# Kernel optimization log

Measured on AMD Instinct MI355X. Metric: run time of the kernel, lower is better.

## Reference

```python
import jax, jax.numpy as jnp
import numpy as np

N_NODES = 100000
N_EDGES = 1600000
D = 128  # in_feats = n_hidden = out_feats


def _linear_params(key, d_in, d_out):
    kw, kb = jax.random.split(key)
    scale = 1.0 / np.sqrt(d_in)
    W = jax.random.uniform(kw, (d_in, d_out), jnp.float32, -scale, scale)
    b = jax.random.uniform(kb, (d_out,), jnp.float32, -scale, scale)
    return W, b


def setup_inputs() -> dict:
    key = jax.random.key(0)
    keys = jax.random.split(key, 8)
    x = jax.random.normal(keys[0], (N_NODES, D), jnp.float32)
    edge_index = jax.random.randint(keys[1], (2, N_EDGES), 0, N_NODES, jnp.int64)
    inp = {"x": x, "edge_index": edge_index}
    for l in range(3):
        W1, b1 = _linear_params(keys[2 + 2 * l], D, D)
        W2, b2 = _linear_params(keys[3 + 2 * l], D, D)
        inp[f"W1_{l}"] = W1
        inp[f"b1_{l}"] = b1
        inp[f"W2_{l}"] = W2
        inp[f"b2_{l}"] = b2
    return inp


def _gin_conv(x, src, dst, W1, b1, W2, b2):
    # GINConv: MLP((1+eps)*x + sum_{j->i} x_j), eps=0
    agg = jax.ops.segment_sum(x[src], dst, num_segments=N_NODES)
    h = agg + x
    h = jnp.maximum(h @ W1 + b1, 0.0)
    return h @ W2 + b2


def reference(x, edge_index, W1_0, b1_0, W2_0, b2_0,
              W1_1, b1_1, W2_1, b2_1, W1_2, b1_2, W2_2, b2_2):
    src, dst = edge_index[0], edge_index[1]
    # layer 0 (loop body): conv -> relu
    x = jnp.maximum(_gin_conv(x, src, dst, W1_0, b1_0, W2_0, b2_0), 0.0)
    # layer 1 (num_layers-2): conv -> relu -> dropout (eval: identity)
    x = jnp.maximum(_gin_conv(x, src, dst, W1_1, b1_1, W2_1, b2_1), 0.0)
    # layer 2 (last): conv -> relu
    x = jnp.maximum(_gin_conv(x, src, dst, W1_2, b1_2, W2_2, b2_2), 0.0)
    return x
```

## Files before the change

kernel.cpp:

```cpp
#include <hip/hip_runtime.h>

#define N_NODES 100000
#define N_EDGES 1600000
#define D 128
#define NBUCK 98
#define CAP 20480
#define PCAP 24576
#define NBLK32 3125

typedef __attribute__((ext_vector_type(8))) short bf16x8;
typedef __attribute__((ext_vector_type(4))) float f32x4;
typedef unsigned long long u64;

__device__ __forceinline__ float b2f_lo(unsigned int u) {
    return __builtin_bit_cast(float, u << 16);
}
__device__ __forceinline__ float b2f_hi(unsigned int u) {
    return __builtin_bit_cast(float, u & 0xFFFF0000u);
}
__device__ __forceinline__ unsigned short f2b(float f) {
    unsigned int u = __builtin_bit_cast(unsigned int, f);
    u += 0x7FFFu + ((u >> 16) & 1u);
    return (unsigned short)(u >> 16);
}


__global__ __launch_bounds__(256) void prep_kernel(
    const float* __restrict__ x, unsigned short* __restrict__ xb,
    const float* __restrict__ W0, const float* __restrict__ W1_, const float* __restrict__ W2_,
    const float* __restrict__ W3, const float* __restrict__ W4, const float* __restrict__ W5,
    unsigned short* __restrict__ T0, unsigned short* __restrict__ T1_,
    unsigned short* __restrict__ T2_, unsigned short* __restrict__ T3,
    unsigned short* __restrict__ T4, unsigned short* __restrict__ T5,
    uint4* __restrict__ dob4, uint4* __restrict__ xs0) {
    int blk = blockIdx.x;
    if (blk < 384) {
        const float* W;
        unsigned short* T;
        switch (blk >> 6) {
            case 0: W = W0; T = T0; break;
            case 1: W = W1_; T = T1_; break;
            case 2: W = W2_; T = T2_; break;
            case 3: W = W3; T = T3; break;
            case 4: W = W4; T = T4; break;
            default: W = W5; T = T5; break;
        }
        int i = (blk & 63) * 256 + threadIdx.x;
        int k = i >> 7, n = i & 127;
        int nt = n >> 4, mr = n & 15;
        int kc = k >> 5, rem = k & 31, quad = rem >> 3, j = rem & 7;
        T[(nt * 4 + kc) * 512 + quad * 128 + mr * 8 + j] = f2b(W[i]);
    } else if (blk < 12884) {
        int i = (blk - 384) * 256 + threadIdx.x;
        if (i < 3200000) {
            float4 v = ((const float4*)x)[i];
            ushort4 o;
            o.x = f2b(v.x); o.y = f2b(v.y); o.z = f2b(v.z); o.w = f2b(v.w);
            ((ushort4*)xb)[i] = o;
        }
    } else {
        int i = (blk - 12884) * 256 + threadIdx.x;
        uint4 z = {0u, 0u, 0u, 0u};
        if (i < 256) dob4[i] = z;
        if (i < 16) xs0[i] = z;
    }
}


__global__ __launch_bounds__(256) void bin_kernel(const int* __restrict__ src,
                                                  const int* __restrict__ dst,
                                                  int* __restrict__ bcur,
                                                  unsigned int* __restrict__ ebuf) {
    __shared__ int h[NBUCK];
    __shared__ int base[NBUCK];
    int tid = threadIdx.x;
    if (tid < NBUCK) h[tid] = 0;
    __syncthreads();
    int e0 = blockIdx.x * 2048;
    int myd[8], mys[8];
#pragma unroll
    for (int i = 0; i < 8; i++) {
        int e = e0 + tid + i * 256;
        int dv = (e < N_EDGES) ? dst[e] : -1;
        myd[i] = dv;
        mys[i] = (e < N_EDGES) ? src[e] : 0;
        if (dv >= 0) atomicAdd(&h[dv >> 10], 1);
    }
    __syncthreads();
    if (tid < NBUCK) {
        int c = h[tid];
        base[tid] = (c > 0) ? (tid * CAP + atomicAdd(&bcur[tid], c)) : 0;
        h[tid] = 0;
    }
    __syncthreads();
#pragma unroll
    for (int i = 0; i < 8; i++) {
        int dv = myd[i];
        if (dv >= 0) {
            int b = dv >> 10;
            int p = base[b] + atomicAdd(&h[b], 1);
            if (p < (b + 1) * CAP)
                ebuf[p] = ((unsigned int)(dv & 1023) << 22) | (unsigned int)mys[i];
        }
    }
}

__global__ __launch_bounds__(1024) void bucket_all_kernel(const unsigned int* __restrict__ ebuf,
                                                          const int* __restrict__ bcur,
                                                          int* __restrict__ off,
                                                          int* __restrict__ offe,
                                                          int* __restrict__ csr) {
    __shared__ int hist[1024];
    __shared__ int sc[1024];
    __shared__ int cnt[1024];
    int b = blockIdx.x, tid = threadIdx.x;
    int nE = bcur[b]; if (nE > CAP) nE = CAP;
    int base = b * PCAP;
    const unsigned int* slab = ebuf + (size_t)b * CAP;
    hist[tid] = 0;
    cnt[tid] = 0;
    __syncthreads();
    for (int i = tid; i < nE; i += 1024)
        atomicAdd(&hist[slab[i] >> 22], 1);
    __syncthreads();
    int node = b * 1024 + tid;
    int d = hist[tid];
    int dp = (node < N_NODES) ? ((d + 3) & ~3) : 0;
    sc[tid] = dp;
    __syncthreads();
#pragma unroll
    for (int s = 1; s < 1024; s <<= 1) {
        int t = (tid >= s) ? sc[tid - s] : 0;
        __syncthreads();
        sc[tid] += t;
        __syncthreads();
    }
    int excl = sc[tid] - dp;
    sc[tid] = excl;
    if (node < N_NODES) {
        off[node] = base + excl;
        offe[node] = base + excl + dp;
    }
    __syncthreads();
    for (int i = tid; i < nE; i += 1024) {
        unsigned int e = slab[i];
        int dd = e >> 22;
        int pos = sc[dd] + atomicAdd(&cnt[dd], 1);
        csr[base + pos] = (int)(e & 0x3FFFFFu);
    }
    for (int j = d; j < dp; j++) csr[base + excl + j] = N_NODES;
}


__global__ __launch_bounds__(256) void agg_bf16(const unsigned int* __restrict__ xb,
                                                const int* __restrict__ off,
                                                const int* __restrict__ offe,
                                                const int* __restrict__ csr,
                                                unsigned int* __restrict__ Pf) {
    int node = blockIdx.x * 4 + (threadIdx.x >> 6);
    int lane = threadIdx.x & 63;
    unsigned int v = xb[(size_t)node * 64 + lane];
    float ax = b2f_lo(v), ay = b2f_hi(v);
    int k = off[node], e = offe[node];
    for (; k + 16 <= e; k += 16) {
        int idx[16];
        unsigned int g[16];
#pragma unroll
        for (int i = 0; i < 16; i++) idx[i] = csr[k + i];
#pragma unroll
        for (int i = 0; i < 16; i++) g[i] = xb[(size_t)idx[i] * 64 + lane];
#pragma unroll
        for (int i = 0; i < 16; i++) { ax += b2f_lo(g[i]); ay += b2f_hi(g[i]); }
    }
    if (k + 8 <= e) {
        int idx[8];
        unsigned int g[8];
#pragma unroll
        for (int i = 0; i < 8; i++) idx[i] = csr[k + i];
#pragma unroll
        for (int i = 0; i < 8; i++) g[i] = xb[(size_t)idx[i] * 64 + lane];
#pragma unroll
        for (int i = 0; i < 8; i++) { ax += b2f_lo(g[i]); ay += b2f_hi(g[i]); }
        k += 8;
    }
    if (k < e) {
        int idx[4];
        unsigned int g[4];
#pragma unroll
        for (int i = 0; i < 4; i++) idx[i] = csr[k + i];
#pragma unroll
        for (int i = 0; i < 4; i++) g[i] = xb[(size_t)idx[i] * 64 + lane];
#pragma unroll
        for (int i = 0; i < 4; i++) { ax += b2f_lo(g[i]); ay += b2f_hi(g[i]); }
    }
    unsigned int packed = (unsigned int)f2b(ax) | ((unsigned int)f2b(ay) << 16);
    int B = node >> 5, sblk = (node >> 4) & 1, mr = node & 15;
    size_t didx = ((size_t)(B * 8 + sblk * 4 + (lane >> 4)) * 64
                   + ((lane >> 2) & 3) * 16 + mr) * 4 + (lane & 3);
    Pf[didx] = packed;
}


template <bool OUT_F32>
__global__ __launch_bounds__(256) void mlp_mfma(const unsigned short* __restrict__ A,
                                                const unsigned short* __restrict__ W1f,
                                                const float* __restrict__ bias1,
                                                const unsigned short* __restrict__ W2f,
                                                const float* __restrict__ bias2,
                                                void* __restrict__ out) {
    __shared__ char smem[4 * 4480];
    int tid = threadIdx.x;
    int wave = tid >> 6, lane = tid & 63;
    int quad = lane >> 4, mr = lane & 15;
    int gw = blockIdx.x * 4 + wave;
    int gwc = (gw > 2 * NBLK32 - 1) ? (2 * NBLK32 - 1) : gw;
    int B = gwc >> 1, sh = gwc & 1;
    int m_base = gw * 16;

    unsigned short* ust = (unsigned short*)(smem + wave * 4480);

    bf16x8 a[4];
#pragma unroll
    for (int kc = 0; kc < 4; kc++)
        a[kc] = *(const bf16x8*)(A + ((size_t)(B * 8 + sh * 4 + kc) * 64 + lane) * 8);

    f32x4 acc[8];
#pragma unroll
    for (int nt = 0; nt < 8; nt++) acc[nt] = (f32x4)0.0f;
#pragma unroll
    for (int nt = 0; nt < 8; nt++) {
#pragma unroll
        for (int kc = 0; kc < 4; kc++) {
            bf16x8 b = *(const bf16x8*)(W1f + (nt * 4 + kc) * 512 + lane * 8);
            acc[nt] = __builtin_amdgcn_mfma_f32_16x16x32_bf16(a[kc], b, acc[nt], 0, 0, 0);
        }
    }
#pragma unroll
    for (int nt = 0; nt < 8; nt++) {
        float bv = bias1[nt * 16 + mr];
#pragma unroll
        for (int r = 0; r < 4; r++)
            ust[(quad * 4 + r) * 136 + nt * 16 + mr] = f2b(fmaxf(acc[nt][r] + bv, 0.0f));
    }

#pragma unroll
    for (int kc = 0; kc < 4; kc++)
        a[kc] = *(const bf16x8*)&ust[mr * 136 + kc * 32 + quad * 8];
#pragma unroll
    for (int nt = 0; nt < 8; nt++) acc[nt] = (f32x4)0.0f;
#pragma unroll
    for (int nt = 0; nt < 8; nt++) {
#pragma unroll
        for (int kc = 0; kc < 4; kc++) {
            bf16x8 b = *(const bf16x8*)(W2f + (nt * 4 + kc) * 512 + lane * 8);
            acc[nt] = __builtin_amdgcn_mfma_f32_16x16x32_bf16(a[kc], b, acc[nt], 0, 0, 0);
        }
    }

    if (OUT_F32) {
        float* st = (float*)ust;
        const int S = 132;
        float* op = (float*)out;
#pragma unroll
        for (int p = 0; p < 2; p++) {
#pragma unroll
            for (int nt = 0; nt < 8; nt++) {
                float bv = bias2[nt * 16 + mr];
#pragma unroll
                for (int r = 0; r < 4; r++) {
                    int row16 = quad * 4 + r;
                    if ((row16 >> 3) == p)
                        st[(row16 & 7) * S + nt * 16 + mr] = fmaxf(acc[nt][r] + bv, 0.0f);
                }
            }
#pragma unroll
            for (int it = 0; it < 4; it++) {
                int linear = lane + it * 64;
                int row = linear >> 5, col = (linear & 31) << 2;
                int gm = m_base + p * 8 + row;
                if (gm < N_NODES) {
                    float4 val = *(float4*)&st[row * S + col];
                    *(float4*)(op + (size_t)gm * D + col) = val;
                }
            }
        }
    } else {
        const int S = 136;
        unsigned short* op = (unsigned short*)out;
#pragma unroll
        for (int nt = 0; nt < 8; nt++) {
            float bv = bias2[nt * 16 + mr];
#pragma unroll
            for (int r = 0; r < 4; r++)
                ust[(quad * 4 + r) * S + nt * 16 + mr] = f2b(fmaxf(acc[nt][r] + bv, 0.0f));
        }
#pragma unroll
        for (int it = 0; it < 4; it++) {
            int linear = lane + it * 64;
            int row = linear >> 4, col = (linear & 15) << 3;
            int gm = m_base + row;
            if (gm < N_NODES) {
                uint4 val = *(uint4*)&ust[row * S + col];
                *(uint4*)(op + (size_t)gm * D + col) = val;
            }
        }
    }
}


extern "C" void kernel_launch(void* const* d_in, const int* in_sizes, int n_in,
                              void* d_out, int out_size, void* d_ws, size_t ws_size,
                              hipStream_t stream) {
    const float* x = (const float*)d_in[0];
    const int* ei = (const int*)d_in[1];
    const int* srcv = ei;
    const int* dstv = ei + N_EDGES;
    const float* W1[3] = {(const float*)d_in[2], (const float*)d_in[6], (const float*)d_in[10]};
    const float* b1[3] = {(const float*)d_in[3], (const float*)d_in[7], (const float*)d_in[11]};
    const float* W2[3] = {(const float*)d_in[4], (const float*)d_in[8], (const float*)d_in[12]};
    const float* b2[3] = {(const float*)d_in[5], (const float*)d_in[9], (const float*)d_in[13]};

    char* ws = (char*)d_ws;
    int* off  = (int*)ws;
    int* offe = (int*)(ws + 400000);
    unsigned short* Wt[6];
    for (int i = 0; i < 6; i++) Wt[i] = (unsigned short*)(ws + 800000 + i * 32768);
    unsigned short* xb = (unsigned short*)(ws + 1048576);
    unsigned short* P  = (unsigned short*)(ws + 26648832);

    char* dob = (char*)d_out;
    int* bcur = (int*)(dob);
    unsigned int* ebuf = (unsigned int*)(dob + 1048576);
    int* csr  = (int*)(dob + 10485760);

    prep_kernel<<<12885, 256, 0, stream>>>(
        x, xb,
        W1[0], W2[0], W1[1], W2[1], W1[2], W2[2],
        Wt[0], Wt[1], Wt[2], Wt[3], Wt[4], Wt[5],
        (uint4*)dob, (uint4*)(xb + (size_t)N_NODES * D));

    bin_kernel<<<782, 256, 0, stream>>>(srcv, dstv, bcur, ebuf);
    bucket_all_kernel<<<NBUCK, 1024, 0, stream>>>(ebuf, bcur, off, offe, csr);

    const int agg_grid = 25000;
    const int mlp_grid = 1563;

    agg_bf16<<<agg_grid, 256, 0, stream>>>((const unsigned int*)xb, off, offe, csr, (unsigned int*)P);
    mlp_mfma<false><<<mlp_grid, 256, 0, stream>>>(P, Wt[0], b1[0], Wt[1], b2[0], xb);
    agg_bf16<<<agg_grid, 256, 0, stream>>>((const unsigned int*)xb, off, offe, csr, (unsigned int*)P);
    mlp_mfma<false><<<mlp_grid, 256, 0, stream>>>(P, Wt[2], b1[1], Wt[3], b2[1], xb);
    agg_bf16<<<agg_grid, 256, 0, stream>>>((const unsigned int*)xb, off, offe, csr, (unsigned int*)P);
    mlp_mfma<true><<<mlp_grid, 256, 0, stream>>>(P, Wt[4], b1[2], Wt[5], b2[2], d_out);
}
```

Baseline: 412.7 us.

## Fuse edge binning into prep kernel, use finer buckets, split aggregation launches

Moves the edge-binning pass into the prep kernel as extra blocks so it overlaps with weight/feature conversion and saves a launch, zeroing bucket counters with a memset. Doubles the number of destination buckets (512 nodes each) so the CSR build runs on more, smaller blocks. Splits each aggregation into two half-size launches over node ranges. The extra launches add overhead and the fused kernel's shared-memory use may lower occupancy for the conversion blocks.

```diff
diff --git a/kernel.cpp b/kernel.cpp
--- a/kernel.cpp
+++ b/kernel.cpp
@@ -3,9 +3,9 @@
 #define N_NODES 100000
 #define N_EDGES 1600000
 #define D 128
-#define NBUCK 98
-#define CAP 20480
-#define PCAP 24576
+#define NBUCK 196
+#define CAP 10240
+#define PCAP 12288
 #define NBLK32 3125
 
 typedef __attribute__((ext_vector_type(8))) short bf16x8;
@@ -32,8 +32,13 @@
     unsigned short* __restrict__ T0, unsigned short* __restrict__ T1_,
     unsigned short* __restrict__ T2_, unsigned short* __restrict__ T3,
     unsigned short* __restrict__ T4, unsigned short* __restrict__ T5,
-    uint4* __restrict__ dob4, uint4* __restrict__ xs0) {
+    const int* __restrict__ src, const int* __restrict__ dst,
+    int* __restrict__ bcur, unsigned int* __restrict__ ebuf,
+    uint4* __restrict__ xs0) {
+    __shared__ int h[NBUCK];
+    __shared__ int hbase[NBUCK];
     int blk = blockIdx.x;
+    int tid = threadIdx.x;
     if (blk < 384) {
         const float* W;
         unsigned short* T;
@@ -45,74 +50,67 @@
             case 4: W = W4; T = T4; break;
             default: W = W5; T = T5; break;
         }
-        int i = (blk & 63) * 256 + threadIdx.x;
+        int i = (blk & 63) * 256 + tid;
         int k = i >> 7, n = i & 127;
         int nt = n >> 4, mr = n & 15;
         int kc = k >> 5, rem = k & 31, quad = rem >> 3, j = rem & 7;
         T[(nt * 4 + kc) * 512 + quad * 128 + mr * 8 + j] = f2b(W[i]);
     } else if (blk < 12884) {
-        int i = (blk - 384) * 256 + threadIdx.x;
+        int i = (blk - 384) * 256 + tid;
         if (i < 3200000) {
             float4 v = ((const float4*)x)[i];
             ushort4 o;
             o.x = f2b(v.x); o.y = f2b(v.y); o.z = f2b(v.z); o.w = f2b(v.w);
             ((ushort4*)xb)[i] = o;
         }
+    } else if (blk < 13666) {
+        int b0 = blk - 12884;
+        if (tid < NBUCK) h[tid] = 0;
+        __syncthreads();
+        int e0 = b0 * 2048;
+        int myd[8], mys[8];
+#pragma unroll
+        for (int i = 0; i < 8; i++) {
+            int e = e0 + tid + i * 256;
+            int dv = (e < N_EDGES) ? dst[e] : -1;
+            myd[i] = dv;
+            mys[i] = (e < N_EDGES) ? src[e] : 0;
+            if (dv >= 0) atomicAdd(&h[dv >> 9], 1);
+        }
+        __syncthreads();
+        if (tid < NBUCK) {
+            int c = h[tid];
+            hbase[tid] = (c > 0) ? (tid * CAP + atomicAdd(&bcur[tid], c)) : 0;
+            h[tid] = 0;
+        }
+        __syncthreads();
+#pragma unroll
+        for (int i = 0; i < 8; i++) {
+            int dv = myd[i];
+            if (dv >= 0) {
+                int b = dv >> 9;
+                int p = hbase[b] + atomicAdd(&h[b], 1);
+                if (p < (b + 1) * CAP)
+                    ebuf[p] = ((unsigned int)(dv & 511) << 22) | (unsigned int)mys[i];
+            }
+        }
     } else {
-        int i = (blk - 12884) * 256 + threadIdx.x;
-        uint4 z = {0u, 0u, 0u, 0u};
-        if (i < 256) dob4[i] = z;
-        if (i < 16) xs0[i] = z;
-    }
-}
-
-
-__global__ __launch_bounds__(256) void bin_kernel(const int* __restrict__ src,
-                                                  const int* __restrict__ dst,
-                                                  int* __restrict__ bcur,
-                                                  unsigned int* __restrict__ ebuf) {
-    __shared__ int h[NBUCK];
-    __shared__ int base[NBUCK];
-    int tid = threadIdx.x;
-    if (tid < NBUCK) h[tid] = 0;
-    __syncthreads();
-    int e0 = blockIdx.x * 2048;
-    int myd[8], mys[8];
-#pragma unroll
-    for (int i = 0; i < 8; i++) {
-        int e = e0 + tid + i * 256;
-        int dv = (e < N_EDGES) ? dst[e] : -1;
-        myd[i] = dv;
-        mys[i] = (e < N_EDGES) ? src[e] : 0;
-        if (dv >= 0) atomicAdd(&h[dv >> 10], 1);
-    }
-    __syncthreads();
-    if (tid < NBUCK) {
-        int c = h[tid];
-        base[tid] = (c > 0) ? (tid * CAP + atomicAdd(&bcur[tid], c)) : 0;
-        h[tid] = 0;
-    }
-    __syncthreads();
-#pragma unroll
-    for (int i = 0; i < 8; i++) {
-        int dv = myd[i];
-        if (dv >= 0) {
-            int b = dv >> 10;
-            int p = base[b] + atomicAdd(&h[b], 1);
-            if (p < (b + 1) * CAP)
-                ebuf[p] = ((unsigned int)(dv & 1023) << 22) | (unsigned int)mys[i];
-        }
-    }
-}
-
-__global__ __launch_bounds__(1024) void bucket_all_kernel(const unsigned int* __restrict__ ebuf,
-                                                          const int* __restrict__ bcur,
-                                                          int* __restrict__ off,
-                                                          int* __restrict__ offe,
-                                                          int* __restrict__ csr) {
-    __shared__ int hist[1024];
-    __shared__ int sc[1024];
-    __shared__ int cnt[1024];
+        if (tid < 16) {
+            uint4 z = {0u, 0u, 0u, 0u};
+            xs0[tid] = z;
+        }
+    }
+}
+
+
+__global__ __launch_bounds__(512) void bucket_all_kernel(const unsigned int* __restrict__ ebuf,
+                                                         const int* __restrict__ bcur,
+                                                         int* __restrict__ off,
+                                                         int* __restrict__ offe,
+                                                         int* __restrict__ csr) {
+    __shared__ int hist[512];
+    __shared__ int sc[512];
+    __shared__ int cnt[512];
     int b = blockIdx.x, tid = threadIdx.x;
     int nE = bcur[b]; if (nE > CAP) nE = CAP;
     int base = b * PCAP;
@@ -120,16 +118,16 @@
     hist[tid] = 0;
     cnt[tid] = 0;
     __syncthreads();
-    for (int i = tid; i < nE; i += 1024)
+    for (int i = tid; i < nE; i += 512)
         atomicAdd(&hist[slab[i] >> 22], 1);
     __syncthreads();
-    int node = b * 1024 + tid;
+    int node = b * 512 + tid;
     int d = hist[tid];
     int dp = (node < N_NODES) ? ((d + 3) & ~3) : 0;
     sc[tid] = dp;
     __syncthreads();
 #pragma unroll
-    for (int s = 1; s < 1024; s <<= 1) {
+    for (int s = 1; s < 512; s <<= 1) {
         int t = (tid >= s) ? sc[tid - s] : 0;
         __syncthreads();
         sc[tid] += t;
@@ -142,7 +140,7 @@
         offe[node] = base + excl + dp;
     }
     __syncthreads();
-    for (int i = tid; i < nE; i += 1024) {
+    for (int i = tid; i < nE; i += 512) {
         unsigned int e = slab[i];
         int dd = e >> 22;
         int pos = sc[dd] + atomicAdd(&cnt[dd], 1);
@@ -156,8 +154,9 @@
                                                 const int* __restrict__ off,
                                                 const int* __restrict__ offe,
                                                 const int* __restrict__ csr,
-                                                unsigned int* __restrict__ Pf) {
-    int node = blockIdx.x * 4 + (threadIdx.x >> 6);
+                                                unsigned int* __restrict__ Pf,
+                                                int nbase) {
+    int node = nbase + blockIdx.x * 4 + (threadIdx.x >> 6);
     int lane = threadIdx.x & 63;
     unsigned int v = xb[(size_t)node * 64 + lane];
     float ax = b2f_lo(v), ay = b2f_hi(v);
@@ -333,22 +332,27 @@
     unsigned int* ebuf = (unsigned int*)(dob + 1048576);
     int* csr  = (int*)(dob + 10485760);
 
-    prep_kernel<<<12885, 256, 0, stream>>>(
+    hipMemsetAsync(bcur, 0, NBUCK * sizeof(int), stream);
+
+    prep_kernel<<<13667, 256, 0, stream>>>(
         x, xb,
         W1[0], W2[0], W1[1], W2[1], W1[2], W2[2],
         Wt[0], Wt[1], Wt[2], Wt[3], Wt[4], Wt[5],
-        (uint4*)dob, (uint4*)(xb + (size_t)N_NODES * D));
-
-    bin_kernel<<<782, 256, 0, stream>>>(srcv, dstv, bcur, ebuf);
-    bucket_all_kernel<<<NBUCK, 1024, 0, stream>>>(ebuf, bcur, off, offe, csr);
-
-    const int agg_grid = 25000;
+        srcv, dstv, bcur, ebuf,
+        (uint4*)(xb + (size_t)N_NODES * D));
+
+    bucket_all_kernel<<<NBUCK, 512, 0, stream>>>(ebuf, bcur, off, offe, csr);
+
+    const int agg_half = 12500;
     const int mlp_grid = 1563;
 
-    agg_bf16<<<agg_grid, 256, 0, stream>>>((const unsigned int*)xb, off, offe, csr, (unsigned int*)P);
+    agg_bf16<<<agg_half, 256, 0, stream>>>((const unsigned int*)xb, off, offe, csr, (unsigned int*)P, 0);
+    agg_bf16<<<agg_half, 256, 0, stream>>>((const unsigned int*)xb, off, offe, csr, (unsigned int*)P, 50000);
     mlp_mfma<false><<<mlp_grid, 256, 0, stream>>>(P, Wt[0], b1[0], Wt[1], b2[0], xb);
-    agg_bf16<<<agg_grid, 256, 0, stream>>>((const unsigned int*)xb, off, offe, csr, (unsigned int*)P);
+    agg_bf16<<<agg_half, 256, 0, stream>>>((const unsigned int*)xb, off, offe, csr, (unsigned int*)P, 0);
+    agg_bf16<<<agg_half, 256, 0, stream>>>((const unsigned int*)xb, off, offe, csr, (unsigned int*)P, 50000);
     mlp_mfma<false><<<mlp_grid, 256, 0, stream>>>(P, Wt[2], b1[1], Wt[3], b2[1], xb);
-    agg_bf16<<<agg_grid, 256, 0, stream>>>((const unsigned int*)xb, off, offe, csr, (unsigned int*)P);
+    agg_bf16<<<agg_half, 256, 0, stream>>>((const unsigned int*)xb, off, offe, csr, (unsigned int*)P, 0);
+    agg_bf16<<<agg_half, 256, 0, stream>>>((const unsigned int*)xb, off, offe, csr, (unsigned int*)P, 50000);
     mlp_mfma<true><<<mlp_grid, 256, 0, stream>>>(P, Wt[4], b1[2], Wt[5], b2[2], d_out);
 }
```

Result: no change. 420.2 us (+1.8%).
